# Performance work log

Hardware: AMD Instinct MI355X
Metric: run time of the kernel (lower is better)

Reference implementation:

```python
import jax, jax.numpy as jnp
import numpy as np

B, T, I, H = 128, 512, 256, 512


def setup_inputs() -> dict:
    key = jax.random.key(0)
    ks = jax.random.split(key, 13)
    s_in = 1.0 / np.sqrt(I)
    s_h = 1.0 / np.sqrt(H)
    return {
        "x": jax.random.normal(ks[0], (B, T, I), jnp.float32),
        "h0": jnp.zeros((B, H), jnp.float32),
        "w_z": jax.random.normal(ks[1], (H, I), jnp.float32) * s_in,
        "w_r": jax.random.normal(ks[2], (H, I), jnp.float32) * s_in,
        "w_h": jax.random.normal(ks[3], (H, I), jnp.float32) * s_in,
        "r_z": jax.random.normal(ks[4], (H, H), jnp.float32) * s_h,
        "r_r": jax.random.normal(ks[5], (H, H), jnp.float32) * s_h,
        "r_h": jax.random.normal(ks[6], (H, H), jnp.float32) * s_h,
        "w_bz": jax.random.normal(ks[7], (H,), jnp.float32) * 0.1,
        "w_br": jax.random.normal(ks[8], (H,), jnp.float32) * 0.1,
        "w_bh": jax.random.normal(ks[9], (H,), jnp.float32) * 0.1,
        "r_bz": jax.random.normal(ks[10], (H,), jnp.float32) * 0.1,
        "r_br": jax.random.normal(ks[11], (H,), jnp.float32) * 0.1,
        "r_bh": jax.random.normal(ks[12], (H,), jnp.float32) * 0.1,
    }


def reference(x, h0, w_z, w_r, w_h, r_z, r_r, r_h,
              w_bz, w_br, w_bh, r_bz, r_br, r_bh):
    # ONNX GRU, linear_before_reset=0, no clip, activations = (sigmoid, tanh).
    # Precompute input-side projections across the whole sequence (same math
    # as per-step matmuls, done once as big GEMMs). Shapes: [B,T,H].
    xz = jnp.einsum('bti,hi->bth', x, w_z) + (w_bz + r_bz)
    xr = jnp.einsum('bti,hi->bth', x, w_r) + (w_br + r_br)
    xh = jnp.einsum('bti,hi->bth', x, w_h) + (w_bh + r_bh)

    # scan over time: carry h [B,H]
    def step(h, xs):
        xz_t, xr_t, xh_t = xs
        z = jax.nn.sigmoid(xz_t + h @ r_z.T)
        r = jax.nn.sigmoid(xr_t + h @ r_r.T)
        hh = jnp.tanh(xh_t + (r * h) @ r_h.T)
        h_new = (1.0 - z) * hh + z * h
        return h_new, h_new

    xs = (jnp.swapaxes(xz, 0, 1), jnp.swapaxes(xr, 0, 1), jnp.swapaxes(xh, 0, 1))
    h_last, seq = jax.lax.scan(step, h0, xs)
    outputs = jnp.swapaxes(seq, 0, 1)  # [B,T,H]
    return outputs, h_last
```

## Files before the change

kernel.cpp:

```cpp
#include <hip/hip_runtime.h>


typedef __attribute__((ext_vector_type(8))) short bf16x8;
typedef __attribute__((ext_vector_type(4))) float f32x4;
typedef unsigned short u16;
typedef unsigned int u32;
typedef unsigned long long u64;

#define B_ 128
#define T_ 512
#define I_ 256
#define H_ 512

__device__ __forceinline__ u16 f2b(float f) {
  union { float f; u32 i; } v; v.f = f;
  u32 u = v.i;
  return (u16)((u + 0x7FFFu + ((u >> 16) & 1u)) >> 16);
}

__device__ __forceinline__ u64 aload(u64* p) {
  return __hip_atomic_load(p, __ATOMIC_RELAXED, __HIP_MEMORY_SCOPE_AGENT);
}
__device__ __forceinline__ void astore(u64* p, u64 v) {
  __hip_atomic_store(p, v, __ATOMIC_RELAXED, __HIP_MEMORY_SCOPE_AGENT);
}

__device__ __forceinline__ void pollwave(u32* f, u32 tgt, int lane) {
  u32 v;
  do {
    v = (lane < 32) ? __hip_atomic_load(&f[lane], __ATOMIC_RELAXED, __HIP_MEMORY_SCOPE_AGENT)
                    : tgt;
  } while (__ballot(v >= tgt) != ~0ull);
  __builtin_amdgcn_s_waitcnt(0);
}

__device__ __forceinline__ void flag_set(u32* p, u32 v) {
  __builtin_amdgcn_s_waitcnt(0);
  __hip_atomic_store(p, v, __ATOMIC_RELAXED, __HIP_MEMORY_SCOPE_AGENT);
}

__global__ void prep_weights(const float* __restrict__ rz, const float* __restrict__ rr,
                             const float* __restrict__ rh, const float* __restrict__ wz,
                             const float* __restrict__ wr, const float* __restrict__ wh,
                             u16* __restrict__ wout) {
  int idx = blockIdx.x * 256 + threadIdx.x;
  if (idx >= 1179648) return;
  float v;
  if (idx < 262144)       v = rz[idx];
  else if (idx < 524288)  v = rr[idx - 262144];
  else if (idx < 786432)  v = rh[idx - 524288];
  else if (idx < 917504)  v = wz[idx - 786432];
  else if (idx < 1048576) v = wr[idx - 917504];
  else                    v = wh[idx - 1048576];
  wout[idx] = f2b(v);
}

__global__ __launch_bounds__(256, 1) void gru_persist(
    const float* __restrict__ x, const float* __restrict__ h0,
    const u16* __restrict__ wsW,
    const float* __restrict__ bwz, const float* __restrict__ bwr, const float* __restrict__ bwh,
    const float* __restrict__ brz, const float* __restrict__ brr, const float* __restrict__ brh,
    float* __restrict__ out, u64* __restrict__ hbq, u64* __restrict__ rhbq,
    u32* __restrict__ flags)
{
  const int tid  = threadIdx.x;
  const int wv   = tid >> 6;
  const int lane = tid & 63;
  const int n    = lane & 15;
  const int q    = lane >> 4;
  const int c    = blockIdx.x >> 3;
  const int w    = blockIdx.x & 7;
  const int nj   = w * 64 + wv * 16 + n;
  const int b0   = c * 16;

  const u16* wrz = wsW;
  const u16* wrr = wsW + 262144;
  const u16* wrh = wsW + 524288;
  const u16* wwz = wsW + 786432;
  const u16* wwr = wsW + 917504;
  const u16* wwh = wsW + 1048576;

  __shared__ __align__(16) u16 sA[16 * 512];
  __shared__ __align__(16) u16 sB[16 * 512];
  __shared__ __align__(16) u16 sX[16 * 256];
  __shared__ __align__(16) u16 sT[4 * 256];

  bf16x8 rzf[16], rrf[16], rhf[16], wzf[8], wrf[8], whf[8];
#pragma unroll
  for (int kb = 0; kb < 16; ++kb) {
    rzf[kb] = *(const bf16x8*)&wrz[nj * H_ + kb * 32 + q * 8];
    rrf[kb] = *(const bf16x8*)&wrr[nj * H_ + kb * 32 + q * 8];
    rhf[kb] = *(const bf16x8*)&wrh[nj * H_ + kb * 32 + q * 8];
  }
#pragma unroll
  for (int kb = 0; kb < 8; ++kb) {
    wzf[kb] = *(const bf16x8*)&wwz[nj * I_ + kb * 32 + q * 8];
    wrf[kb] = *(const bf16x8*)&wwr[nj * I_ + kb * 32 + q * 8];
    whf[kb] = *(const bf16x8*)&wwh[nj * I_ + kb * 32 + q * 8];
  }

  const float bz  = bwz[nj] + brz[nj];
  const float brg = bwr[nj] + brr[nj];
  const float bhg = bwh[nj] + brh[nj];

  float hold[4];
#pragma unroll
  for (int i = 0; i < 4; ++i) hold[i] = h0[(b0 + q * 4 + i) * H_ + nj];

  u32* hf = flags + c * 64;
  u32* rf = flags + c * 64 + 32;
  const int myflag = w * 4 + wv;

  const int prow = lane >> 2, pcq = lane & 3;
  const int pubidx = ((b0 + prow) * H_ + w * 64 + wv * 16 + pcq * 4) >> 2;
  u16* sTw = &sT[wv * 256];

  {
#pragma unroll
    for (int i = 0; i < 4; ++i) sTw[(q * 4 + i) * 16 + n] = f2b(hold[i]);
    __threadfence_block();
    astore(&hbq[pubidx], *(const u64*)&sTw[prow * 16 + pcq * 4]);
    if (lane == 0) flag_set(&hf[myflag], 1u);
    else __builtin_amdgcn_s_waitcnt(0);
  }

  for (int t = 0; t < T_; ++t) {
    __syncthreads();

#pragma unroll
    for (int it = 0; it < 2; ++it) {
      int id = it * 256 + tid;
      int row = id >> 5, kc = id & 31;
      const float* src = &x[(b0 + row) * (T_ * I_) + t * I_ + kc * 8];
      float4 v0 = *(const float4*)src;
      float4 v1 = *(const float4*)(src + 4);
      union { u16 u[8]; bf16x8 v; } pk;
      pk.u[0] = f2b(v0.x); pk.u[1] = f2b(v0.y); pk.u[2] = f2b(v0.z); pk.u[3] = f2b(v0.w);
      pk.u[4] = f2b(v1.x); pk.u[5] = f2b(v1.y); pk.u[6] = f2b(v1.z); pk.u[7] = f2b(v1.w);
      *(bf16x8*)&sX[row * 256 + (kc ^ (row & 7)) * 8] = pk.v;
    }

    pollwave(hf, (u32)(t + 1), lane);
#pragma unroll
    for (int it = 0; it < 4; ++it) {
      int id = it * 256 + tid;
      int row = id >> 6, kc = id & 63;
      int base = ((b0 + row) * H_ + kc * 8) >> 2;
      union { u64 qd[2]; bf16x8 v; } u;
      u.qd[0] = aload(&hbq[base]);
      u.qd[1] = aload(&hbq[base + 1]);
      *(bf16x8*)&sA[row * 512 + (kc ^ (row & 7)) * 8] = u.v;
    }
    __syncthreads();

    f32x4 az0 = {0.f,0.f,0.f,0.f}, az1 = {0.f,0.f,0.f,0.f};
    f32x4 ar0 = {0.f,0.f,0.f,0.f}, ar1 = {0.f,0.f,0.f,0.f};
#pragma unroll
    for (int kb = 0; kb < 16; kb += 2) {
      bf16x8 a0 = *(const bf16x8*)&sA[n * 512 + ((kb * 4 + q) ^ (n & 7)) * 8];
      az0 = __builtin_amdgcn_mfma_f32_16x16x32_bf16(a0, rzf[kb], az0, 0, 0, 0);
      ar0 = __builtin_amdgcn_mfma_f32_16x16x32_bf16(a0, rrf[kb], ar0, 0, 0, 0);
      bf16x8 a1 = *(const bf16x8*)&sA[n * 512 + (((kb + 1) * 4 + q) ^ (n & 7)) * 8];
      az1 = __builtin_amdgcn_mfma_f32_16x16x32_bf16(a1, rzf[kb + 1], az1, 0, 0, 0);
      ar1 = __builtin_amdgcn_mfma_f32_16x16x32_bf16(a1, rrf[kb + 1], ar1, 0, 0, 0);
    }
#pragma unroll
    for (int kb = 0; kb < 8; kb += 2) {
      bf16x8 a0 = *(const bf16x8*)&sX[n * 256 + ((kb * 4 + q) ^ (n & 7)) * 8];
      az0 = __builtin_amdgcn_mfma_f32_16x16x32_bf16(a0, wzf[kb], az0, 0, 0, 0);
      ar0 = __builtin_amdgcn_mfma_f32_16x16x32_bf16(a0, wrf[kb], ar0, 0, 0, 0);
      bf16x8 a1 = *(const bf16x8*)&sX[n * 256 + (((kb + 1) * 4 + q) ^ (n & 7)) * 8];
      az1 = __builtin_amdgcn_mfma_f32_16x16x32_bf16(a1, wzf[kb + 1], az1, 0, 0, 0);
      ar1 = __builtin_amdgcn_mfma_f32_16x16x32_bf16(a1, wrf[kb + 1], ar1, 0, 0, 0);
    }

    float zreg[4];
#pragma unroll
    for (int i = 0; i < 4; ++i) {
      zreg[i] = 1.f / (1.f + __expf(-(az0[i] + az1[i] + bz)));
      float rv = 1.f / (1.f + __expf(-(ar0[i] + ar1[i] + brg)));
      sTw[(q * 4 + i) * 16 + n] = f2b(rv * hold[i]);
    }
    __threadfence_block();
    astore(&rhbq[pubidx], *(const u64*)&sTw[prow * 16 + pcq * 4]);
    if (lane == 0) flag_set(&rf[myflag], (u32)(t + 1));

    f32x4 ah0 = {0.f,0.f,0.f,0.f}, ah1 = {0.f,0.f,0.f,0.f};
#pragma unroll
    for (int kb = 0; kb < 8; kb += 2) {
      bf16x8 a0 = *(const bf16x8*)&sX[n * 256 + ((kb * 4 + q) ^ (n & 7)) * 8];
      ah0 = __builtin_amdgcn_mfma_f32_16x16x32_bf16(a0, whf[kb], ah0, 0, 0, 0);
      bf16x8 a1 = *(const bf16x8*)&sX[n * 256 + (((kb + 1) * 4 + q) ^ (n & 7)) * 8];
      ah1 = __builtin_amdgcn_mfma_f32_16x16x32_bf16(a1, whf[kb + 1], ah1, 0, 0, 0);
    }

    pollwave(rf, (u32)(t + 1), lane);
#pragma unroll
    for (int it = 0; it < 4; ++it) {
      int id = it * 256 + tid;
      int row = id >> 6, kc = id & 63;
      int base = ((b0 + row) * H_ + kc * 8) >> 2;
      union { u64 qd[2]; bf16x8 v; } u;
      u.qd[0] = aload(&rhbq[base]);
      u.qd[1] = aload(&rhbq[base + 1]);
      *(bf16x8*)&sB[row * 512 + (kc ^ (row & 7)) * 8] = u.v;
    }
    __syncthreads();

#pragma unroll
    for (int kb = 0; kb < 16; kb += 2) {
      bf16x8 a0 = *(const bf16x8*)&sB[n * 512 + ((kb * 4 + q) ^ (n & 7)) * 8];
      ah0 = __builtin_amdgcn_mfma_f32_16x16x32_bf16(a0, rhf[kb], ah0, 0, 0, 0);
      bf16x8 a1 = *(const bf16x8*)&sB[n * 512 + (((kb + 1) * 4 + q) ^ (n & 7)) * 8];
      ah1 = __builtin_amdgcn_mfma_f32_16x16x32_bf16(a1, rhf[kb + 1], ah1, 0, 0, 0);
    }

#pragma unroll
    for (int i = 0; i < 4; ++i) {
      float hhv = tanhf(ah0[i] + ah1[i] + bhg);
      float hn  = (1.f - zreg[i]) * hhv + zreg[i] * hold[i];
      hold[i] = hn;
      out[(b0 + q * 4 + i) * (T_ * H_) + t * H_ + nj] = hn;
      if (t == T_ - 1) out[B_ * T_ * H_ + (b0 + q * 4 + i) * H_ + nj] = hn;
      sTw[(q * 4 + i) * 16 + n] = f2b(hn);
    }
    __threadfence_block();
    astore(&hbq[pubidx], *(const u64*)&sTw[prow * 16 + pcq * 4]);
    if (lane == 0) flag_set(&hf[myflag], (u32)(t + 2));
  }
}

extern "C" void kernel_launch(void* const* d_in, const int* in_sizes, int n_in,
                              void* d_out, int out_size, void* d_ws, size_t ws_size,
                              hipStream_t stream) {
  const float* xp   = (const float*)d_in[0];
  const float* h0p  = (const float*)d_in[1];
  const float* wzp  = (const float*)d_in[2];
  const float* wrp  = (const float*)d_in[3];
  const float* whp  = (const float*)d_in[4];
  const float* rzp  = (const float*)d_in[5];
  const float* rrp  = (const float*)d_in[6];
  const float* rhp  = (const float*)d_in[7];
  const float* bwzp = (const float*)d_in[8];
  const float* bwrp = (const float*)d_in[9];
  const float* bwhp = (const float*)d_in[10];
  const float* brzp = (const float*)d_in[11];
  const float* brrp = (const float*)d_in[12];
  const float* brhp = (const float*)d_in[13];

  unsigned char* ws = (unsigned char*)d_ws;
  u16* wsW  = (u16*)(ws);
  u64* hbq  = (u64*)(ws + 2359296);
  u64* rhbq = (u64*)(ws + 2490368);
  u32* flags = (u32*)(ws + 2621440);

  hipMemsetAsync(ws + 2621440, 0, 4096, stream);

  prep_weights<<<dim3(4608), dim3(256), 0, stream>>>(rzp, rrp, rhp, wzp, wrp, whp, wsW);

  gru_persist<<<dim3(64), dim3(256), 0, stream>>>(
      xp, h0p, wsW,
      bwzp, bwrp, bwhp, brzp, brrp, brhp,
      (float*)d_out, hbq, rhbq, flags);
}
```

Baseline: 4.100 ms.

## Replace flag polling with step-tagged data words in the inter-block exchange

```diff
diff --git a/kernel.cpp b/kernel.cpp
--- a/kernel.cpp
+++ b/kernel.cpp
@@ -22,20 +22,6 @@
   return __hip_atomic_load(p, __ATOMIC_RELAXED, __HIP_MEMORY_SCOPE_AGENT);
 }
 __device__ __forceinline__ void astore(u64* p, u64 v) {
-  __hip_atomic_store(p, v, __ATOMIC_RELAXED, __HIP_MEMORY_SCOPE_AGENT);
-}
-
-__device__ __forceinline__ void pollwave(u32* f, u32 tgt, int lane) {
-  u32 v;
-  do {
-    v = (lane < 32) ? __hip_atomic_load(&f[lane], __ATOMIC_RELAXED, __HIP_MEMORY_SCOPE_AGENT)
-                    : tgt;
-  } while (__ballot(v >= tgt) != ~0ull);
-  __builtin_amdgcn_s_waitcnt(0);
-}
-
-__device__ __forceinline__ void flag_set(u32* p, u32 v) {
-  __builtin_amdgcn_s_waitcnt(0);
   __hip_atomic_store(p, v, __ATOMIC_RELAXED, __HIP_MEMORY_SCOPE_AGENT);
 }
 
@@ -55,13 +41,52 @@
   wout[idx] = f2b(v);
 }
 
+__device__ __forceinline__ void gather_panel(u64* __restrict__ buf, int b0, int tid,
+                                             u32 tg, u16* __restrict__ dst) {
+  u64 qd[16];
+  u64* pA[4];
+  int rowA[4], kcA[4];
+#pragma unroll
+  for (int it = 0; it < 4; ++it) {
+    int id  = it * 256 + tid;
+    int row = id >> 6, kc = id & 63;
+    rowA[it] = row; kcA[it] = kc;
+    u64* p = buf + (((b0 + row) * H_ + kc * 8) >> 1);
+    pA[it] = p;
+    qd[it * 4 + 0] = aload(p);
+    qd[it * 4 + 1] = aload(p + 1);
+    qd[it * 4 + 2] = aload(p + 2);
+    qd[it * 4 + 3] = aload(p + 3);
+  }
+#pragma unroll
+  for (int it = 0; it < 4; ++it) {
+    for (;;) {
+      bool ok = true;
+#pragma unroll
+      for (int k2 = 0; k2 < 4; ++k2) {
+        u64 v = qd[it * 4 + k2];
+        ok &= (((v >> 16) & 0xFFFFu) == tg) & ((u32)(v >> 48) == tg);
+      }
+      if (__builtin_expect(ok, 1)) break;
+#pragma unroll
+      for (int k2 = 0; k2 < 4; ++k2) qd[it * 4 + k2] = aload(pA[it] + k2);
+    }
+    union { u32 w[4]; bf16x8 v; } pk;
+#pragma unroll
+    for (int k2 = 0; k2 < 4; ++k2) {
+      u64 v = qd[it * 4 + k2];
+      pk.w[k2] = (u32)(v & 0xFFFFu) | ((u32)((v >> 32) & 0xFFFFu) << 16);
+    }
+    *(bf16x8*)&dst[rowA[it] * 512 + (kcA[it] ^ (rowA[it] & 7)) * 8] = pk.v;
+  }
+}
+
 __global__ __launch_bounds__(256, 1) void gru_persist(
     const float* __restrict__ x, const float* __restrict__ h0,
     const u16* __restrict__ wsW,
     const float* __restrict__ bwz, const float* __restrict__ bwr, const float* __restrict__ bwh,
     const float* __restrict__ brz, const float* __restrict__ brr, const float* __restrict__ brh,
-    float* __restrict__ out, u64* __restrict__ hbq, u64* __restrict__ rhbq,
-    u32* __restrict__ flags)
+    float* __restrict__ out, u64* __restrict__ hbt, u64* __restrict__ rhbt)
 {
   const int tid  = threadIdx.x;
   const int wv   = tid >> 6;
@@ -83,7 +108,7 @@
   __shared__ __align__(16) u16 sA[16 * 512];
   __shared__ __align__(16) u16 sB[16 * 512];
   __shared__ __align__(16) u16 sX[16 * 256];
-  __shared__ __align__(16) u16 sT[4 * 256];
+  __shared__ __align__(16) u32 sT[4 * 256];
 
   bf16x8 rzf[16], rrf[16], rhf[16], wzf[8], wrf[8], whf[8];
 #pragma unroll
@@ -107,24 +132,21 @@
 #pragma unroll
   for (int i = 0; i < 4; ++i) hold[i] = h0[(b0 + q * 4 + i) * H_ + nj];
 
-  u32* hf = flags + c * 64;
-  u32* rf = flags + c * 64 + 32;
-  const int myflag = w * 4 + wv;
-
-  const int prow = lane >> 2, pcq = lane & 3;
-  const int pubidx = ((b0 + prow) * H_ + w * 64 + wv * 16 + pcq * 4) >> 2;
-  u16* sTw = &sT[wv * 256];
+  const int prow = lane >> 2, pc0 = (lane & 3) * 4;
+  const int pub64 = (((b0 + prow) * H_ + w * 64 + wv * 16 + pc0) >> 1);
+  u32* sTw = &sT[wv * 256];
 
   {
 #pragma unroll
-    for (int i = 0; i < 4; ++i) sTw[(q * 4 + i) * 16 + n] = f2b(hold[i]);
+    for (int i = 0; i < 4; ++i)
+      sTw[(q * 4 + i) * 16 + n] = (1u << 16) | (u32)f2b(hold[i]);
     __threadfence_block();
-    astore(&hbq[pubidx], *(const u64*)&sTw[prow * 16 + pcq * 4]);
-    if (lane == 0) flag_set(&hf[myflag], 1u);
-    else __builtin_amdgcn_s_waitcnt(0);
+    astore(&hbt[pub64],     *(const u64*)&sTw[prow * 16 + pc0]);
+    astore(&hbt[pub64 + 1], *(const u64*)&sTw[prow * 16 + pc0 + 2]);
   }
 
   for (int t = 0; t < T_; ++t) {
+    const u32 tg = (u32)(t + 1);
     __syncthreads();
 
 #pragma unroll
@@ -140,17 +162,7 @@
       *(bf16x8*)&sX[row * 256 + (kc ^ (row & 7)) * 8] = pk.v;
     }
 
-    pollwave(hf, (u32)(t + 1), lane);
-#pragma unroll
-    for (int it = 0; it < 4; ++it) {
-      int id = it * 256 + tid;
-      int row = id >> 6, kc = id & 63;
-      int base = ((b0 + row) * H_ + kc * 8) >> 2;
-      union { u64 qd[2]; bf16x8 v; } u;
-      u.qd[0] = aload(&hbq[base]);
-      u.qd[1] = aload(&hbq[base + 1]);
-      *(bf16x8*)&sA[row * 512 + (kc ^ (row & 7)) * 8] = u.v;
-    }
+    gather_panel(hbt, b0, tid, tg, sA);
     __syncthreads();
 
     f32x4 az0 = {0.f,0.f,0.f,0.f}, az1 = {0.f,0.f,0.f,0.f};
@@ -179,11 +191,11 @@
     for (int i = 0; i < 4; ++i) {
       zreg[i] = 1.f / (1.f + __expf(-(az0[i] + az1[i] + bz)));
       float rv = 1.f / (1.f + __expf(-(ar0[i] + ar1[i] + brg)));
-      sTw[(q * 4 + i) * 16 + n] = f2b(rv * hold[i]);
+      sTw[(q * 4 + i) * 16 + n] = (tg << 16) | (u32)f2b(rv * hold[i]);
     }
     __threadfence_block();
-    astore(&rhbq[pubidx], *(const u64*)&sTw[prow * 16 + pcq * 4]);
-    if (lane == 0) flag_set(&rf[myflag], (u32)(t + 1));
+    astore(&rhbt[pub64],     *(const u64*)&sTw[prow * 16 + pc0]);
+    astore(&rhbt[pub64 + 1], *(const u64*)&sTw[prow * 16 + pc0 + 2]);
 
     f32x4 ah0 = {0.f,0.f,0.f,0.f}, ah1 = {0.f,0.f,0.f,0.f};
 #pragma unroll
@@ -194,17 +206,7 @@
       ah1 = __builtin_amdgcn_mfma_f32_16x16x32_bf16(a1, whf[kb + 1], ah1, 0, 0, 0);
     }
 
-    pollwave(rf, (u32)(t + 1), lane);
-#pragma unroll
-    for (int it = 0; it < 4; ++it) {
-      int id = it * 256 + tid;
-      int row = id >> 6, kc = id & 63;
-      int base = ((b0 + row) * H_ + kc * 8) >> 2;
-      union { u64 qd[2]; bf16x8 v; } u;
-      u.qd[0] = aload(&rhbq[base]);
-      u.qd[1] = aload(&rhbq[base + 1]);
-      *(bf16x8*)&sB[row * 512 + (kc ^ (row & 7)) * 8] = u.v;
-    }
+    gather_panel(rhbt, b0, tid, tg, sB);
     __syncthreads();
 
 #pragma unroll
@@ -215,18 +217,22 @@
       ah1 = __builtin_amdgcn_mfma_f32_16x16x32_bf16(a1, rhf[kb + 1], ah1, 0, 0, 0);
     }
 
+    float hn4[4];
 #pragma unroll
     for (int i = 0; i < 4; ++i) {
       float hhv = tanhf(ah0[i] + ah1[i] + bhg);
       float hn  = (1.f - zreg[i]) * hhv + zreg[i] * hold[i];
-      hold[i] = hn;
-      out[(b0 + q * 4 + i) * (T_ * H_) + t * H_ + nj] = hn;
-      if (t == T_ - 1) out[B_ * T_ * H_ + (b0 + q * 4 + i) * H_ + nj] = hn;
-      sTw[(q * 4 + i) * 16 + n] = f2b(hn);
+      hold[i] = hn; hn4[i] = hn;
+      sTw[(q * 4 + i) * 16 + n] = ((tg + 1u) << 16) | (u32)f2b(hn);
     }
     __threadfence_block();
-    astore(&hbq[pubidx], *(const u64*)&sTw[prow * 16 + pcq * 4]);
-    if (lane == 0) flag_set(&hf[myflag], (u32)(t + 2));
+    astore(&hbt[pub64],     *(const u64*)&sTw[prow * 16 + pc0]);
+    astore(&hbt[pub64 + 1], *(const u64*)&sTw[prow * 16 + pc0 + 2]);
+#pragma unroll
+    for (int i = 0; i < 4; ++i) {
+      out[(b0 + q * 4 + i) * (T_ * H_) + t * H_ + nj] = hn4[i];
+      if (t == T_ - 1) out[B_ * T_ * H_ + (b0 + q * 4 + i) * H_ + nj] = hn4[i];
+    }
   }
 }
 
@@ -250,16 +256,13 @@
 
   unsigned char* ws = (unsigned char*)d_ws;
   u16* wsW  = (u16*)(ws);
-  u64* hbq  = (u64*)(ws + 2359296);
-  u64* rhbq = (u64*)(ws + 2490368);
-  u32* flags = (u32*)(ws + 2621440);
-
-  hipMemsetAsync(ws + 2621440, 0, 4096, stream);
+  u64* hbt  = (u64*)(ws + 2359296);
+  u64* rhbt = (u64*)(ws + 2621440);
 
   prep_weights<<<dim3(4608), dim3(256), 0, stream>>>(rzp, rrp, rhp, wzp, wrp, whp, wsW);
 
   gru_persist<<<dim3(64), dim3(256), 0, stream>>>(
       xp, h0p, wsW,
       bwzp, bwrp, bwhp, brzp, brrp, brhp,
-      (float*)d_out, hbq, rhbq, flags);
-}
+      (float*)d_out, hbt, rhbt);
+}
```

Result: slower. 4.190 ms (+2.2%).
